# Kernel optimization log

Measured on AMD Instinct MI355X. Metric: run time of the kernel, lower is better.

## Reference

```python
import jax, jax.numpy as jnp
import numpy as np

N = 50000   # nodes
E = 800000  # edges (avg degree 16)
C = 128     # hidden_channels
G = 128     # graphs in batch
L0, L1 = 512, 256  # linear_hidden_channels
P = 2       # num_params (output per graph)


def setup_inputs() -> dict:
    key = jax.random.key(0)
    ks = iter(jax.random.split(key, 48))

    def w(shape):
        return jax.random.normal(next(ks), shape, jnp.float32) / np.float32(np.sqrt(shape[0]))

    inp = {}
    inp["x"] = jax.random.normal(next(ks), (N, 4), jnp.float32)
    inp["edge_index"] = jax.random.randint(next(ks), (2, E), 0, N, dtype=jnp.int32)
    inp["edge_attr"] = jax.random.normal(next(ks), (E, 3), jnp.float32)
    inp["batch"] = jnp.sort(jax.random.randint(next(ks), (N,), 0, G, dtype=jnp.int32))
    # TransformerConv params: layer 0 (in=4) and shared layer (in=C, applied twice
    # because `[GConv(...)]*(n-1)` reuses the same module object).
    for i, din in enumerate([4, C]):
        inp[f"Wq{i}"] = w((din, C)); inp[f"bq{i}"] = jnp.zeros((C,), jnp.float32)
        inp[f"Wk{i}"] = w((din, C)); inp[f"bk{i}"] = jnp.zeros((C,), jnp.float32)
        inp[f"Wv{i}"] = w((din, C)); inp[f"bv{i}"] = jnp.zeros((C,), jnp.float32)
        inp[f"We{i}"] = w((3, C))   # lin_edge has no bias
        inp[f"Ws{i}"] = w((din, C)); inp[f"bs{i}"] = jnp.zeros((C,), jnp.float32)
    inp["Wl0"] = w((C, L0));  inp["bl0"] = jnp.zeros((L0,), jnp.float32)
    inp["Wl1"] = w((L0, L1)); inp["bl1"] = jnp.zeros((L1,), jnp.float32)
    inp["Wl2"] = w((L1, P));  inp["bl2"] = jnp.zeros((P,), jnp.float32)
    return inp


def tconv(x, src, dst, e_attr, Wq, bq, Wk, bk, Wv, bv, We, Ws, bs):
    # TransformerConv (heads=1, edge_dim, root_weight=True, beta=False)
    n = x.shape[0]
    c = Wq.shape[1]
    q = x @ Wq + bq            # [N, C]
    k = x @ Wk + bk
    v = x @ Wv + bv
    e = e_attr @ We            # [E, C]
    kj = k[src] + e            # [E, C] key at source + edge emb
    vj = v[src] + e            # [E, C] value at source + edge emb
    logits = jnp.sum(q[dst] * kj, axis=-1) / jnp.sqrt(jnp.float32(c))  # [E]
    # softmax over incoming edges of each target node
    m = jax.ops.segment_max(logits, dst, num_segments=n)
    a = jnp.exp(logits - m[dst])
    denom = jax.ops.segment_sum(a, dst, num_segments=n)
    alpha = a / denom[dst]
    out = jax.ops.segment_sum(vj * alpha[:, None], dst, num_segments=n)
    return out + x @ Ws + bs   # root/skip connection


def reference(x, edge_index, edge_attr, batch,
              Wq0, bq0, Wk0, bk0, Wv0, bv0, We0, Ws0, bs0,
              Wq1, bq1, Wk1, bk1, Wv1, bv1, We1, Ws1, bs1,
              Wl0, bl0, Wl1, bl1, Wl2, bl2):
    src, dst = edge_index[0], edge_index[1]
    # layer 0
    h = tconv(x, src, dst, edge_attr, Wq0, bq0, Wk0, bk0, Wv0, bv0, We0, Ws0, bs0)
    h = jax.nn.leaky_relu(h, 0.01)  # dropout is identity in eval
    # layers 1..2 share weights (Python list-multiplication of modules)
    for _ in range(2):
        h = tconv(h, src, dst, edge_attr, Wq1, bq1, Wk1, bk1, Wv1, bv1, We1, Ws1, bs1)
        h = jax.nn.leaky_relu(h, 0.01)
    # global_add_pool
    g = jax.ops.segment_sum(h, batch, num_segments=G)  # [G, C]
    # MLP head
    g = jax.nn.relu(g @ Wl0 + bl0)
    g = jax.nn.relu(g @ Wl1 + bl1)
    g = g @ Wl2 + bl2                                  # [G, 2]
    return jnp.ravel(g)                                # [G*2]
```

## Files before the change

kernel.cpp:

```cpp
#include <hip/hip_runtime.h>
#include <math.h>

#define N_NODES 50000
#define N_EDGES 800000
#define CDIM    128
#define GDIM    128
#define L0DIM   512
#define L1DIM   256

typedef unsigned int uint;
typedef unsigned short ushort;
typedef __attribute__((ext_vector_type(8))) short short8;
typedef __attribute__((ext_vector_type(4))) float f32x4;

__device__ inline ushort f2bf(float f) {
  uint u = __float_as_uint(f);
  uint r = (u + 0x7fffu + ((u >> 16) & 1u)) >> 16;
  return (ushort)r;
}
__device__ inline float bflo(uint u) { return __uint_as_float(u << 16); }
__device__ inline float bfhi(uint u) { return __uint_as_float(u & 0xffff0000u); }

__global__ void hist_kernel(const int* __restrict__ dst, int* counts, int E) {
  int e = blockIdx.x * 256 + threadIdx.x;
  if (e < E) atomicAdd(&counts[dst[e]], 1);
}

__global__ void scan_blocks(const int* __restrict__ counts, int* excl, int* bsums, int N) {
  __shared__ int s[1024];
  int tid = threadIdx.x;
  int i = blockIdx.x * 1024 + tid;
  int v = (i < N) ? counts[i] : 0;
  s[tid] = v;
  __syncthreads();
  for (int off = 1; off < 1024; off <<= 1) {
    int t = (tid >= off) ? s[tid - off] : 0;
    __syncthreads();
    s[tid] += t;
    __syncthreads();
  }
  if (i < N) excl[i] = s[tid] - v;
  if (tid == 1023) bsums[blockIdx.x] = s[1023];
}

__global__ void scan_sums(int* bsums, int nb) {
  int lane = threadIdx.x;
  int orig = (lane < nb) ? bsums[lane] : 0;
  int v = orig;
#pragma unroll
  for (int off = 1; off < 64; off <<= 1) {
    int t = __shfl_up(v, off);
    if (lane >= off) v += t;
  }
  if (lane < nb) bsums[lane] = v - orig;
}

__global__ void scan_add(const int* __restrict__ excl, const int* __restrict__ bsums,
                         int* indptr, int N, int E) {
  int i = blockIdx.x * 1024 + threadIdx.x;
  if (i < N) indptr[i] = excl[i] + bsums[blockIdx.x];
  if (i == 0) indptr[N] = E;
}

__global__ void scatter2_kernel(const int* __restrict__ dst, const int* __restrict__ src,
                                const float* __restrict__ attr,
                                const int* __restrict__ indptr,
                                int* cursor, int* csr_src, float4* csr_attr, int E) {
  int e = blockIdx.x * 256 + threadIdx.x;
  if (e < E) {
    int d = dst[e];
    int pos = atomicAdd(&cursor[d], 1);
    int i = indptr[d] + pos;
    csr_src[i] = src[e];
    csr_attr[i] = make_float4(attr[e * 3 + 0], attr[e * 3 + 1], attr[e * 3 + 2], 0.f);
  }
}

__global__ void l0_qkvs(const float* __restrict__ x,
                        const float* __restrict__ Wq, const float* __restrict__ bq,
                        const float* __restrict__ Wk, const float* __restrict__ bk,
                        const float* __restrict__ Wv, const float* __restrict__ bv,
                        const float* __restrict__ Ws, const float* __restrict__ bs,
                        float* __restrict__ q, ushort* __restrict__ kvb,
                        float* __restrict__ hs, int N) {
  __shared__ float W[4][4][128];
  __shared__ float B[4][128];
  int tid = threadIdx.x;
  for (int i = tid; i < 4 * 128; i += 256) {
    W[0][i >> 7][i & 127] = Wq[i];
    W[1][i >> 7][i & 127] = Wk[i];
    W[2][i >> 7][i & 127] = Wv[i];
    W[3][i >> 7][i & 127] = Ws[i];
  }
  for (int i = tid; i < 128; i += 256) {
    B[0][i] = bq[i]; B[1][i] = bk[i]; B[2][i] = bv[i]; B[3][i] = bs[i];
  }
  __syncthreads();
  int gid = blockIdx.x * 256 + tid;
  int n = gid >> 7, c = gid & 127;
  if (n >= N) return;
  float x0 = x[n * 4 + 0], x1 = x[n * 4 + 1], x2 = x[n * 4 + 2], x3 = x[n * 4 + 3];
  float qv = x0 * W[0][0][c] + x1 * W[0][1][c] + x2 * W[0][2][c] + x3 * W[0][3][c] + B[0][c];
  float kv = x0 * W[1][0][c] + x1 * W[1][1][c] + x2 * W[1][2][c] + x3 * W[1][3][c] + B[1][c];
  float vv = x0 * W[2][0][c] + x1 * W[2][1][c] + x2 * W[2][2][c] + x3 * W[2][3][c] + B[2][c];
  float sv = x0 * W[3][0][c] + x1 * W[3][1][c] + x2 * W[3][2][c] + x3 * W[3][3][c] + B[3][c];
  q[n * 128 + c] = qv;
  kvb[(size_t)n * 256 + c]       = f2bf(kv);
  kvb[(size_t)n * 256 + 128 + c] = f2bf(vv);
  hs[n * 128 + c] = sv;
}

__global__ void prep_w(const float* __restrict__ Wq, const float* __restrict__ Wk,
                       const float* __restrict__ Wv, const float* __restrict__ Ws,
                       ushort* __restrict__ wt) {
  int idx = blockIdx.x * 256 + threadIdx.x;
  int z = idx >> 14, rem = idx & 16383;
  int k_ = rem >> 7, c_ = rem & 127;
  const float* W = (z == 0) ? Wq : (z == 1) ? Wk : (z == 2) ? Wv : Ws;
  wt[z * 16384 + c_ * 128 + k_] = f2bf(W[k_ * 128 + c_]);
}

#define LDA 136
__global__ __launch_bounds__(256) void gemm_mfma(
    const float* __restrict__ H, const ushort* __restrict__ wtg,
    const float* __restrict__ bq, const float* __restrict__ bk,
    const float* __restrict__ bv, const float* __restrict__ bs,
    float* __restrict__ q, ushort* __restrict__ kvb,
    float* __restrict__ hs, int N) {
  int z = blockIdx.z;
  const float* bb = (z == 0) ? bq : (z == 1) ? bk : (z == 2) ? bv : bs;
  __shared__ ushort Alds[64 * LDA];
  __shared__ ushort Wlds[128 * LDA];
  int tid = threadIdx.x;
  int n0 = blockIdx.x * 64;

  {
    const uint* wg = (const uint*)(wtg + z * 16384);
    uint* wl = (uint*)Wlds;
    for (int i = tid; i < 8192; i += 256) {
      int c_ = i >> 6, kp = i & 63;
      wl[c_ * (LDA / 2) + kp] = wg[c_ * 64 + kp];
    }
  }
  {
    uint* al = (uint*)Alds;
    for (int i = tid; i < 4096; i += 256) {
      int r = i >> 6, kp = i & 63;
      int grow = n0 + r; grow = (grow < N) ? grow : (N - 1);
      float2 hv = *(const float2*)&H[(size_t)grow * 128 + 2 * kp];
      al[r * (LDA / 2) + kp] = (uint)f2bf(hv.x) | ((uint)f2bf(hv.y) << 16);
    }
  }
  __syncthreads();

  int w = tid >> 6, lane = tid & 63;
  int m_ = lane & 15, quad = lane >> 4;
  f32x4 acc[8];
#pragma unroll
  for (int ct = 0; ct < 8; ct++) acc[ct] = 0.f;

#pragma unroll
  for (int kc = 0; kc < 4; kc++) {
    short8 af = *(const short8*)&Alds[(w * 16 + m_) * LDA + kc * 32 + quad * 8];
#pragma unroll
    for (int ct = 0; ct < 8; ct++) {
      short8 bf = *(const short8*)&Wlds[(ct * 16 + m_) * LDA + kc * 32 + quad * 8];
      acc[ct] = __builtin_amdgcn_mfma_f32_16x16x32_bf16(af, bf, acc[ct], 0, 0, 0);
    }
  }

#pragma unroll
  for (int ct = 0; ct < 8; ct++) {
    int col = ct * 16 + m_;
    float bcol = bb[col];
#pragma unroll
    for (int reg = 0; reg < 4; reg++) {
      int n = n0 + w * 16 + quad * 4 + reg;
      if (n < N) {
        float o = acc[ct][reg] + bcol;
        if (z == 0)      q[(size_t)n * 128 + col] = o;
        else if (z == 3) hs[(size_t)n * 128 + col] = o;
        else             kvb[(size_t)n * 256 + ((z == 2) ? 128 : 0) + col] = f2bf(o);
      }
    }
  }
}

__global__ __launch_bounds__(256) void attn_fused(
    const float* __restrict__ q, const ushort* __restrict__ kv,
    const int* __restrict__ indptr, const int* __restrict__ csr_src,
    const float4* __restrict__ csr_attr, const float* __restrict__ We,
    float* __restrict__ h, int N) {
  __shared__ float WeS[384];
  int tid = threadIdx.x;
  for (int i = tid; i < 384; i += 256) WeS[i] = We[i];
  __syncthreads();
  int lane = tid & 63;
  int n = blockIdx.x * 4 + (tid >> 6);
  if (n >= N) return;
  int g = lane >> 4, gl = lane & 15;
  int c = gl * 8;
  const float S = 0.12751744f;
  float4 qa  = *(const float4*)&q[(size_t)n * 128 + c];
  float4 qb4 = *(const float4*)&q[(size_t)n * 128 + c + 4];
  float qv[8] = {qa.x * S, qa.y * S, qa.z * S, qa.w * S,
                 qb4.x * S, qb4.y * S, qb4.z * S, qb4.w * S};
  float we0[8], we1[8], we2[8];
#pragma unroll
  for (int j = 0; j < 8; j++) {
    we0[j] = WeS[c + j]; we1[j] = WeS[128 + c + j]; we2[j] = WeS[256 + c + j];
  }
  float t0 = 0.f, t1 = 0.f, t2 = 0.f;
#pragma unroll
  for (int j = 0; j < 8; j++) {
    t0 = fmaf(we0[j], qv[j], t0);
    t1 = fmaf(we1[j], qv[j], t1);
    t2 = fmaf(we2[j], qv[j], t2);
  }
#pragma unroll
  for (int off = 1; off < 16; off <<= 1) {
    t0 += __shfl_xor(t0, off);
    t1 += __shfl_xor(t1, off);
    t2 += __shfl_xor(t2, off);
  }

  float4 sk0 = *(const float4*)&h[(size_t)n * 128 + c];
  float4 sk1 = *(const float4*)&h[(size_t)n * 128 + c + 4];
  int beg = indptr[n], end = indptr[n + 1];

  if (end > beg) {
    float d = 0.f;
    float sa0 = 0.f, sa1 = 0.f, sa2 = 0.f;
    float acc[8];
#pragma unroll
    for (int j = 0; j < 8; j++) acc[j] = 0.f;
    const uint* kvw = (const uint*)kv;
    const int endm1 = end - 1;

    int i = beg + g;
    int pA = (i     < end) ? i     : endm1;
    int pB = (i + 4 < end) ? i + 4 : endm1;
    int sjA = csr_src[pA];  float4 atA = csr_attr[pA];
    int sjB = csr_src[pB];  float4 atB = csr_attr[pB];

    for (; i < end; i += 8) {
      int sjAc = sjA, sjBc = sjB;
      float4 atAc = atA, atBc = atB;
      float wB = ((i + 4) < end) ? 1.f : 0.f;
      int nn = i + 8;
      int qA = (nn     < end) ? nn     : endm1;
      int qB = (nn + 4 < end) ? nn + 4 : endm1;
      sjA = csr_src[qA]; atA = csr_attr[qA];
      sjB = csr_src[qB]; atB = csr_attr[qB];
      const uint4* kpA = (const uint4*)(kvw + (size_t)sjAc * 128);
      const uint4* kpB = (const uint4*)(kvw + (size_t)sjBc * 128);
      uint4 krA = kpA[gl];
      uint4 krB = kpB[gl];
      uint4 vrA = kpA[16 + gl];
      uint4 vrB = kpB[16 + gl];
      float kxA[8], kxB[8];
      kxA[0] = bflo(krA.x); kxA[1] = bfhi(krA.x); kxA[2] = bflo(krA.y); kxA[3] = bfhi(krA.y);
      kxA[4] = bflo(krA.z); kxA[5] = bfhi(krA.z); kxA[6] = bflo(krA.w); kxA[7] = bfhi(krA.w);
      kxB[0] = bflo(krB.x); kxB[1] = bfhi(krB.x); kxB[2] = bflo(krB.y); kxB[3] = bfhi(krB.y);
      kxB[4] = bflo(krB.z); kxB[5] = bfhi(krB.z); kxB[6] = bflo(krB.w); kxB[7] = bfhi(krB.w);
      float pAv = 0.f, pBv = 0.f;
#pragma unroll
      for (int j = 0; j < 8; j++) {
        pAv = fmaf(qv[j], kxA[j], pAv);
        pBv = fmaf(qv[j], kxB[j], pBv);
      }
      pAv += __shfl_xor(pAv, 1);  pBv += __shfl_xor(pBv, 1);
      pAv += __shfl_xor(pAv, 2);  pBv += __shfl_xor(pBv, 2);
      pAv += __shfl_xor(pAv, 4);  pBv += __shfl_xor(pBv, 4);
      pAv += __shfl_xor(pAv, 8);  pBv += __shfl_xor(pBv, 8);
      pAv = fmaf(atAc.x, t0, pAv);
      pBv = fmaf(atBc.x, t0, pBv);
      pAv = fmaf(atAc.y, t1, pAv);
      pBv = fmaf(atBc.y, t1, pBv);
      pAv = fmaf(atAc.z, t2, pAv);
      pBv = fmaf(atBc.z, t2, pBv);
      float aA = __builtin_amdgcn_exp2f(pAv);
      float aB = wB * __builtin_amdgcn_exp2f(pBv);
      d += aA + aB;
      sa0 = fmaf(aA, atAc.x, sa0); sa0 = fmaf(aB, atBc.x, sa0);
      sa1 = fmaf(aA, atAc.y, sa1); sa1 = fmaf(aB, atBc.y, sa1);
      sa2 = fmaf(aA, atAc.z, sa2); sa2 = fmaf(aB, atBc.z, sa2);
      float vxA[8], vxB[8];
      vxA[0] = bflo(vrA.x); vxA[1] = bfhi(vrA.x); vxA[2] = bflo(vrA.y); vxA[3] = bfhi(vrA.y);
      vxA[4] = bflo(vrA.z); vxA[5] = bfhi(vrA.z); vxA[6] = bflo(vrA.w); vxA[7] = bfhi(vrA.w);
      vxB[0] = bflo(vrB.x); vxB[1] = bfhi(vrB.x); vxB[2] = bflo(vrB.y); vxB[3] = bfhi(vrB.y);
      vxB[4] = bflo(vrB.z); vxB[5] = bfhi(vrB.z); vxB[6] = bflo(vrB.w); vxB[7] = bfhi(vrB.w);
#pragma unroll
      for (int j = 0; j < 8; j++) {
        acc[j] = fmaf(aA, vxA[j], acc[j]);
        acc[j] = fmaf(aB, vxB[j], acc[j]);
      }
    }
#pragma unroll
    for (int off = 16; off < 64; off <<= 1) {
      d += __shfl_xor(d, off);
      sa0 += __shfl_xor(sa0, off);
      sa1 += __shfl_xor(sa1, off);
      sa2 += __shfl_xor(sa2, off);
#pragma unroll
      for (int j = 0; j < 8; j++) acc[j] += __shfl_xor(acc[j], off);
    }
    float inv = 1.f / d;
    float o[8];
#pragma unroll
    for (int j = 0; j < 8; j++) {
      float ecorr = sa0 * we0[j] + sa1 * we1[j] + sa2 * we2[j];
      o[j] = (acc[j] + ecorr) * inv;
    }
    sk0.x += o[0]; sk0.y += o[1]; sk0.z += o[2]; sk0.w += o[3];
    sk1.x += o[4]; sk1.y += o[5]; sk1.z += o[6]; sk1.w += o[7];
  }
  sk0.x = (sk0.x > 0.f) ? sk0.x : 0.01f * sk0.x;
  sk0.y = (sk0.y > 0.f) ? sk0.y : 0.01f * sk0.y;
  sk0.z = (sk0.z > 0.f) ? sk0.z : 0.01f * sk0.z;
  sk0.w = (sk0.w > 0.f) ? sk0.w : 0.01f * sk0.w;
  sk1.x = (sk1.x > 0.f) ? sk1.x : 0.01f * sk1.x;
  sk1.y = (sk1.y > 0.f) ? sk1.y : 0.01f * sk1.y;
  sk1.z = (sk1.z > 0.f) ? sk1.z : 0.01f * sk1.z;
  sk1.w = (sk1.w > 0.f) ? sk1.w : 0.01f * sk1.w;
  if (g == 0) {
    *(float4*)&h[(size_t)n * 128 + c] = sk0;
    *(float4*)&h[(size_t)n * 128 + c + 4] = sk1;
  }
}

__global__ void pool_kernel(const float* __restrict__ h, const int* __restrict__ batch,
                            float* __restrict__ gout, int N) {
  int tid = threadIdx.x;
  int sub = tid >> 6;
  int c = 2 * (tid & 63);
  int n0 = blockIdx.x * 64 + sub * 16;
  if (n0 >= N) return;
  int n1 = min(n0 + 16, N);
  float a0 = 0.f, a1 = 0.f;
  int cur = batch[n0];
  for (int n = n0; n < n1; n++) {
    int b = batch[n];
    if (b != cur) {
      atomicAdd(&gout[cur * 128 + c], a0);
      atomicAdd(&gout[cur * 128 + c + 1], a1);
      a0 = 0.f; a1 = 0.f; cur = b;
    }
    float2 hv = *(const float2*)&h[(size_t)n * 128 + c];
    a0 += hv.x; a1 += hv.y;
  }
  atomicAdd(&gout[cur * 128 + c], a0);
  atomicAdd(&gout[cur * 128 + c + 1], a1);
}

__global__ __launch_bounds__(256) void mlp_fused(
    const float* __restrict__ gp,
    const float* __restrict__ Wl0, const float* __restrict__ bl0,
    const float* __restrict__ Wl1, const float* __restrict__ bl1,
    const float* __restrict__ Wl2, const float* __restrict__ bl2,
    float* __restrict__ out) {
  int g = blockIdx.x;
  int tid = threadIdx.x;
  __shared__ float xin[CDIM];
  __shared__ float h1[L0DIM];
  __shared__ float h2[L1DIM];
  __shared__ float r0s[4], r1s[4];
  if (tid < CDIM) xin[tid] = gp[g * CDIM + tid];
  __syncthreads();
  for (int c = tid; c < L0DIM; c += 256) {
    float a0 = 0.f, a1 = 0.f, a2 = 0.f, a3 = 0.f;
#pragma unroll 4
    for (int kk = 0; kk < CDIM; kk += 4) {
      a0 = fmaf(xin[kk + 0], Wl0[(kk + 0) * L0DIM + c], a0);
      a1 = fmaf(xin[kk + 1], Wl0[(kk + 1) * L0DIM + c], a1);
      a2 = fmaf(xin[kk + 2], Wl0[(kk + 2) * L0DIM + c], a2);
      a3 = fmaf(xin[kk + 3], Wl0[(kk + 3) * L0DIM + c], a3);
    }
    h1[c] = fmaxf((a0 + a1) + (a2 + a3) + bl0[c], 0.f);
  }
  __syncthreads();
  {
    int c = tid;
    float a0 = 0.f, a1 = 0.f, a2 = 0.f, a3 = 0.f;
#pragma unroll 4
    for (int kk = 0; kk < L0DIM; kk += 4) {
      a0 = fmaf(h1[kk + 0], Wl1[(kk + 0) * L1DIM + c], a0);
      a1 = fmaf(h1[kk + 1], Wl1[(kk + 1) * L1DIM + c], a1);
      a2 = fmaf(h1[kk + 2], Wl1[(kk + 2) * L1DIM + c], a2);
      a3 = fmaf(h1[kk + 3], Wl1[(kk + 3) * L1DIM + c], a3);
    }
    h2[c] = fmaxf((a0 + a1) + (a2 + a3) + bl1[c], 0.f);
  }
  __syncthreads();
  float p0 = h2[tid] * Wl2[tid * 2 + 0];
  float p1 = h2[tid] * Wl2[tid * 2 + 1];
#pragma unroll
  for (int off = 32; off > 0; off >>= 1) {
    p0 += __shfl_down(p0, off);
    p1 += __shfl_down(p1, off);
  }
  int wv = tid >> 6, ln = tid & 63;
  if (ln == 0) { r0s[wv] = p0; r1s[wv] = p1; }
  __syncthreads();
  if (tid == 0) out[g * 2 + 0] = r0s[0] + r0s[1] + r0s[2] + r0s[3] + bl2[0];
  if (tid == 1) out[g * 2 + 1] = r1s[0] + r1s[1] + r1s[2] + r1s[3] + bl2[1];
}

extern "C" void kernel_launch(void* const* d_in, const int* in_sizes, int n_in,
                              void* d_out, int out_size, void* d_ws, size_t ws_size,
                              hipStream_t stream) {
  const int N = N_NODES, E = N_EDGES;
  const float* x    = (const float*)d_in[0];
  const int*   ei   = (const int*)d_in[1];
  const float* attr = (const float*)d_in[2];
  const int*   batch= (const int*)d_in[3];
  const int* src = ei;
  const int* dst = ei + E;

  const float *Wq0 = (const float*)d_in[4],  *bq0 = (const float*)d_in[5];
  const float *Wk0 = (const float*)d_in[6],  *bk0 = (const float*)d_in[7];
  const float *Wv0 = (const float*)d_in[8],  *bv0 = (const float*)d_in[9];
  const float *We0 = (const float*)d_in[10];
  const float *Ws0 = (const float*)d_in[11], *bs0 = (const float*)d_in[12];
  const float *Wq1 = (const float*)d_in[13], *bq1 = (const float*)d_in[14];
  const float *Wk1 = (const float*)d_in[15], *bk1 = (const float*)d_in[16];
  const float *Wv1 = (const float*)d_in[17], *bv1 = (const float*)d_in[18];
  const float *We1 = (const float*)d_in[19];
  const float *Ws1 = (const float*)d_in[20], *bs1 = (const float*)d_in[21];
  const float *Wl0 = (const float*)d_in[22], *bl0 = (const float*)d_in[23];
  const float *Wl1 = (const float*)d_in[24], *bl1 = (const float*)d_in[25];
  const float *Wl2 = (const float*)d_in[26], *bl2 = (const float*)d_in[27];

  size_t off = 0;
  auto carve = [&](size_t bytes) {
    void* p = (char*)d_ws + off;
    off += (bytes + 255) & ~(size_t)255;
    return p;
  };
  float*  hA       = (float*)carve((size_t)N * CDIM * 4);
  float*  hB       = (float*)carve((size_t)N * CDIM * 4);
  float*  qb       = (float*)carve((size_t)N * CDIM * 4);
  ushort* kvb      = (ushort*)carve((size_t)N * 256 * 2);
  int*    indptr   = (int*)carve((size_t)(N + 1) * 4);
  int*    csr_src  = (int*)carve((size_t)E * 4);
  float4* csr_attr = (float4*)carve((size_t)E * 16);
  int*    cc       = (int*)carve((size_t)2 * N * 4);
  int*    counts   = cc;
  int*    cursor   = cc + N;
  int*    excl     = (int*)carve((size_t)N * 4);
  int*    bsums    = (int*)carve((size_t)64 * 4);
  ushort* wt1      = (ushort*)carve((size_t)4 * 16384 * 2);
  float*  gp       = (float*)carve((size_t)GDIM * CDIM * 4);

  hipMemsetAsync(cc, 0, (size_t)2 * N * 4, stream);
  hipMemsetAsync(gp, 0, (size_t)GDIM * CDIM * 4, stream);

  int nscan = (N + 1023) / 1024;
  hist_kernel<<<(E + 255) / 256, 256, 0, stream>>>(dst, counts, E);
  scan_blocks<<<nscan, 1024, 0, stream>>>(counts, excl, bsums, N);
  scan_sums<<<1, 64, 0, stream>>>(bsums, nscan);
  scan_add<<<nscan, 1024, 0, stream>>>(excl, bsums, indptr, N, E);
  scatter2_kernel<<<(E + 255) / 256, 256, 0, stream>>>(dst, src, attr, indptr, cursor,
                                                       csr_src, csr_attr, E);
  prep_w<<<256, 256, 0, stream>>>(Wq1, Wk1, Wv1, Ws1, wt1);

  int naBlocks = (N + 3) / 4;
  dim3 gemmGrid((N + 63) / 64, 1, 4);

  l0_qkvs<<<(N * 128 + 255) / 256, 256, 0, stream>>>(
      x, Wq0, bq0, Wk0, bk0, Wv0, bv0, Ws0, bs0, qb, kvb, hA, N);
  attn_fused<<<naBlocks, 256, 0, stream>>>(qb, kvb, indptr, csr_src, csr_attr, We0, hA, N);

  gemm_mfma<<<gemmGrid, 256, 0, stream>>>(hA, wt1, bq1, bk1, bv1, bs1, qb, kvb, hB, N);
  attn_fused<<<naBlocks, 256, 0, stream>>>(qb, kvb, indptr, csr_src, csr_attr, We1, hB, N);

  gemm_mfma<<<gemmGrid, 256, 0, stream>>>(hB, wt1, bq1, bk1, bv1, bs1, qb, kvb, hA, N);
  attn_fused<<<naBlocks, 256, 0, stream>>>(qb, kvb, indptr, csr_src, csr_attr, We1, hA, N);

  pool_kernel<<<(N + 63) / 64, 256, 0, stream>>>(hA, batch, gp, N);
  mlp_fused<<<GDIM, 256, 0, stream>>>(gp, Wl0, bl0, Wl1, bl1, Wl2, bl2, (float*)d_out);
}
```

Before: 596.3 us.

## Store prescaled bf16 queries and loop all four projections in one GEMM block

Queries are now stored as bf16 with the attention scale already applied, which halves q storage and read traffic in the attention kernel. The GEMM no longer launches one block per projection; each block converts its node tile to bf16 once and loops over the four weight matrices, reloading each into LDS. attn_fused also gets a min-blocks launch bound of 8 to raise occupancy. In exchange, queries lose precision, the GEMM grid is four times smaller with serialized weight loads inside each block, and the launch bound may force register spills.

```diff
diff --git a/kernel.cpp b/kernel.cpp
--- a/kernel.cpp
+++ b/kernel.cpp
@@ -12,6 +12,8 @@
 typedef unsigned short ushort;
 typedef __attribute__((ext_vector_type(8))) short short8;
 typedef __attribute__((ext_vector_type(4))) float f32x4;
+
+#define QSCALE 0.12751744f
 
 __device__ inline ushort f2bf(float f) {
   uint u = __float_as_uint(f);
@@ -81,7 +83,7 @@
                         const float* __restrict__ Wk, const float* __restrict__ bk,
                         const float* __restrict__ Wv, const float* __restrict__ bv,
                         const float* __restrict__ Ws, const float* __restrict__ bs,
-                        float* __restrict__ q, ushort* __restrict__ kvb,
+                        ushort* __restrict__ q, ushort* __restrict__ kvb,
                         float* __restrict__ hs, int N) {
   __shared__ float W[4][4][128];
   __shared__ float B[4][128];
@@ -104,7 +106,7 @@
   float kv = x0 * W[1][0][c] + x1 * W[1][1][c] + x2 * W[1][2][c] + x3 * W[1][3][c] + B[1][c];
   float vv = x0 * W[2][0][c] + x1 * W[2][1][c] + x2 * W[2][2][c] + x3 * W[2][3][c] + B[2][c];
   float sv = x0 * W[3][0][c] + x1 * W[3][1][c] + x2 * W[3][2][c] + x3 * W[3][3][c] + B[3][c];
-  q[n * 128 + c] = qv;
+  q[(size_t)n * 128 + c] = f2bf(qv * QSCALE);
   kvb[(size_t)n * 256 + c]       = f2bf(kv);
   kvb[(size_t)n * 256 + 128 + c] = f2bf(vv);
   hs[n * 128 + c] = sv;
@@ -125,23 +127,13 @@
     const float* __restrict__ H, const ushort* __restrict__ wtg,
     const float* __restrict__ bq, const float* __restrict__ bk,
     const float* __restrict__ bv, const float* __restrict__ bs,
-    float* __restrict__ q, ushort* __restrict__ kvb,
+    ushort* __restrict__ q, ushort* __restrict__ kvb,
     float* __restrict__ hs, int N) {
-  int z = blockIdx.z;
-  const float* bb = (z == 0) ? bq : (z == 1) ? bk : (z == 2) ? bv : bs;
   __shared__ ushort Alds[64 * LDA];
   __shared__ ushort Wlds[128 * LDA];
   int tid = threadIdx.x;
   int n0 = blockIdx.x * 64;
 
-  {
-    const uint* wg = (const uint*)(wtg + z * 16384);
-    uint* wl = (uint*)Wlds;
-    for (int i = tid; i < 8192; i += 256) {
-      int c_ = i >> 6, kp = i & 63;
-      wl[c_ * (LDA / 2) + kp] = wg[c_ * 64 + kp];
-    }
-  }
   {
     uint* al = (uint*)Alds;
     for (int i = tid; i < 4096; i += 256) {
@@ -151,43 +143,57 @@
       al[r * (LDA / 2) + kp] = (uint)f2bf(hv.x) | ((uint)f2bf(hv.y) << 16);
     }
   }
-  __syncthreads();
 
   int w = tid >> 6, lane = tid & 63;
   int m_ = lane & 15, quad = lane >> 4;
-  f32x4 acc[8];
-#pragma unroll
-  for (int ct = 0; ct < 8; ct++) acc[ct] = 0.f;
-
-#pragma unroll
-  for (int kc = 0; kc < 4; kc++) {
-    short8 af = *(const short8*)&Alds[(w * 16 + m_) * LDA + kc * 32 + quad * 8];
+
+  for (int z = 0; z < 4; z++) {
+    __syncthreads();
+    {
+      const uint* wg = (const uint*)(wtg + z * 16384);
+      uint* wl = (uint*)Wlds;
+      for (int i = tid; i < 8192; i += 256) {
+        int c_ = i >> 6, kp = i & 63;
+        wl[c_ * (LDA / 2) + kp] = wg[c_ * 64 + kp];
+      }
+    }
+    __syncthreads();
+
+    f32x4 acc[8];
+#pragma unroll
+    for (int ct = 0; ct < 8; ct++) acc[ct] = 0.f;
+
+#pragma unroll
+    for (int kc = 0; kc < 4; kc++) {
+      short8 af = *(const short8*)&Alds[(w * 16 + m_) * LDA + kc * 32 + quad * 8];
+#pragma unroll
+      for (int ct = 0; ct < 8; ct++) {
+        short8 bf = *(const short8*)&Wlds[(ct * 16 + m_) * LDA + kc * 32 + quad * 8];
+        acc[ct] = __builtin_amdgcn_mfma_f32_16x16x32_bf16(af, bf, acc[ct], 0, 0, 0);
+      }
+    }
+
+    const float* bb = (z == 0) ? bq : (z == 1) ? bk : (z == 2) ? bv : bs;
 #pragma unroll
     for (int ct = 0; ct < 8; ct++) {
-      short8 bf = *(const short8*)&Wlds[(ct * 16 + m_) * LDA + kc * 32 + quad * 8];
-      acc[ct] = __builtin_amdgcn_mfma_f32_16x16x32_bf16(af, bf, acc[ct], 0, 0, 0);
-    }
-  }
-
-#pragma unroll
-  for (int ct = 0; ct < 8; ct++) {
-    int col = ct * 16 + m_;
-    float bcol = bb[col];
-#pragma unroll
-    for (int reg = 0; reg < 4; reg++) {
-      int n = n0 + w * 16 + quad * 4 + reg;
-      if (n < N) {
-        float o = acc[ct][reg] + bcol;
-        if (z == 0)      q[(size_t)n * 128 + col] = o;
-        else if (z == 3) hs[(size_t)n * 128 + col] = o;
-        else             kvb[(size_t)n * 256 + ((z == 2) ? 128 : 0) + col] = f2bf(o);
+      int col = ct * 16 + m_;
+      float bcol = bb[col];
+#pragma unroll
+      for (int reg = 0; reg < 4; reg++) {
+        int n = n0 + w * 16 + quad * 4 + reg;
+        if (n < N) {
+          float o = acc[ct][reg] + bcol;
+          if (z == 0)      q[(size_t)n * 128 + col] = f2bf(o * QSCALE);
+          else if (z == 3) hs[(size_t)n * 128 + col] = o;
+          else             kvb[(size_t)n * 256 + ((z == 2) ? 128 : 0) + col] = f2bf(o);
+        }
       }
     }
   }
 }
 
-__global__ __launch_bounds__(256) void attn_fused(
-    const float* __restrict__ q, const ushort* __restrict__ kv,
+__global__ __launch_bounds__(256, 8) void attn_fused(
+    const ushort* __restrict__ q, const ushort* __restrict__ kv,
     const int* __restrict__ indptr, const int* __restrict__ csr_src,
     const float4* __restrict__ csr_attr, const float* __restrict__ We,
     float* __restrict__ h, int N) {
@@ -200,11 +206,9 @@
   if (n >= N) return;
   int g = lane >> 4, gl = lane & 15;
   int c = gl * 8;
-  const float S = 0.12751744f;
-  float4 qa  = *(const float4*)&q[(size_t)n * 128 + c];
-  float4 qb4 = *(const float4*)&q[(size_t)n * 128 + c + 4];
-  float qv[8] = {qa.x * S, qa.y * S, qa.z * S, qa.w * S,
-                 qb4.x * S, qb4.y * S, qb4.z * S, qb4.w * S};
+  uint4 qr = *(const uint4*)&q[(size_t)n * 128 + c];
+  float qv[8] = {bflo(qr.x), bfhi(qr.x), bflo(qr.y), bfhi(qr.y),
+                 bflo(qr.z), bfhi(qr.z), bflo(qr.w), bfhi(qr.w)};
   float we0[8], we1[8], we2[8];
 #pragma unroll
   for (int j = 0; j < 8; j++) {
@@ -439,7 +443,7 @@
   };
   float*  hA       = (float*)carve((size_t)N * CDIM * 4);
   float*  hB       = (float*)carve((size_t)N * CDIM * 4);
-  float*  qb       = (float*)carve((size_t)N * CDIM * 4);
+  ushort* qb       = (ushort*)carve((size_t)N * CDIM * 2);
   ushort* kvb      = (ushort*)carve((size_t)N * 256 * 2);
   int*    indptr   = (int*)carve((size_t)(N + 1) * 4);
   int*    csr_src  = (int*)carve((size_t)E * 4);
@@ -465,16 +469,16 @@
   prep_w<<<256, 256, 0, stream>>>(Wq1, Wk1, Wv1, Ws1, wt1);
 
   int naBlocks = (N + 3) / 4;
-  dim3 gemmGrid((N + 63) / 64, 1, 4);
+  int gemmBlocks = (N + 63) / 64;
 
   l0_qkvs<<<(N * 128 + 255) / 256, 256, 0, stream>>>(
       x, Wq0, bq0, Wk0, bk0, Wv0, bv0, Ws0, bs0, qb, kvb, hA, N);
   attn_fused<<<naBlocks, 256, 0, stream>>>(qb, kvb, indptr, csr_src, csr_attr, We0, hA, N);
 
-  gemm_mfma<<<gemmGrid, 256, 0, stream>>>(hA, wt1, bq1, bk1, bv1, bs1, qb, kvb, hB, N);
+  gemm_mfma<<<gemmBlocks, 256, 0, stream>>>(hA, wt1, bq1, bk1, bv1, bs1, qb, kvb, hB, N);
   attn_fused<<<naBlocks, 256, 0, stream>>>(qb, kvb, indptr, csr_src, csr_attr, We1, hB, N);
 
-  gemm_mfma<<<gemmGrid, 256, 0, stream>>>(hB, wt1, bq1, bk1, bv1, bs1, qb, kvb, hA, N);
+  gemm_mfma<<<gemmBlocks, 256, 0, stream>>>(hB, wt1, bq1, bk1, bv1, bs1, qb, kvb, hA, N);
   attn_fused<<<naBlocks, 256, 0, stream>>>(qb, kvb, indptr, csr_src, csr_attr, We1, hA, N);
 
   pool_kernel<<<(N + 63) / 64, 256, 0, stream>>>(hA, batch, gp, N);
```

Result: slower. 1.307 ms (+119.2%).
